# Kernel tuning notes

Hardware: AMD Instinct MI355X
Metric: run time of the kernel (lower is better)

Reference implementation:

```python
import jax, jax.numpy as jnp
import numpy as np

HEADS, DIM_HEAD = 8, 75            # Attention defaults in source
SCALE = DIM_HEAD ** -0.5
NUM_FOURIER = 64
PATCH = 4


def scale_norm(x, g, eps=1e-5):
    n = jnp.maximum(jnp.linalg.norm(x, axis=-1, keepdims=True), eps)
    return x / n * g


def attention(x, ctx, mask, wq, wkv, wo, bo):
    b, nq, _ = x.shape
    q = (x @ wq).reshape(b, nq, HEADS, DIM_HEAD)
    k, v = jnp.split(ctx @ wkv, 2, axis=-1)
    k = k.reshape(b, -1, HEADS, DIM_HEAD)
    v = v.reshape(b, -1, HEADS, DIM_HEAD)
    sim = jnp.einsum('bihd,bjhd->bhij', q, k) * SCALE
    if mask is not None:
        sim = jnp.where(mask[:, None, None, :], sim, -jnp.finfo(sim.dtype).max)
    a = jax.nn.softmax(sim, axis=-1)
    out = jnp.einsum('bhij,bjhd->bihd', a, v).reshape(b, nq, HEADS * DIM_HEAD)
    return out @ wo + bo


def feedforward(x, w1, b1, w2, b2):
    return jax.nn.gelu(x @ w1 + b1, approximate=False) @ w2 + b2


def fourier_encode(x, num_encodings):
    xu = x[..., None]
    scales = (2.0 ** jnp.arange(num_encodings)).astype(x.dtype)
    xs = xu / scales
    return jnp.concatenate([jnp.sin(xs), jnp.cos(xs), xu], axis=-1)


def sparsify(x, threshold=0.3):
    # x: (b, h, w, nt, c) patched volume. Fixed max_len = h*w*nt; stable sort
    # compacts kept voxels to the front in row-major (y,x,t) order, matching
    # torch.where ordering. Padded slots are zeroed and masked out.
    b, h, w, nt, c = x.shape
    N = h * w * nt
    mask = (jnp.abs(jnp.max(x, axis=-1)) > threshold).reshape(b, N)
    ys, xs, ts = jnp.meshgrid(jnp.arange(h), jnp.arange(w), jnp.arange(nt), indexing='ij')
    pos = jnp.stack([2.0 * ys / h - 1.0, 2.0 * xs / w - 1.0, 2.0 * ts / nt - 1.0], -1)
    pos = pos.reshape(N, 3).astype(x.dtype)
    order = jnp.argsort((~mask).astype(jnp.int32), axis=1)  # jax sort is stable
    mask_s = jnp.take_along_axis(mask, order, axis=1)
    pos_s = pos[order] * mask_s[..., None]
    vals_s = jnp.take_along_axis(x.reshape(b, N, c), order[..., None], axis=1) * mask_s[..., None]
    return pos_s, vals_s, mask_s


def _forward(input, latents, pos_emb,
             ca_g, ca_ctx_g, ca_q, ca_kv, ca_ow, ca_ob,
             cf_g, cf_w1, cf_b1, cf_w2, cf_b2,
             la_g, la_q, la_kv, la_ow, la_ob,
             lf_g, lf_w1, lf_b1, lf_w2, lf_b2,
             logits_w, logits_b):
    num_tbins = input.shape[0]
    x = jnp.transpose(input, (1, 3, 4, 0, 2))  # b h w t c
    b, H, W, t, c = x.shape
    p = PATCH
    x = x.reshape(b, H // p, p, W // p, p, t, c)
    x = jnp.transpose(x, (0, 1, 3, 5, 2, 4, 6)).reshape(b, H // p, W // p, t, p * p * c)
    pos, vals, mask = sparsify(x)
    enc = fourier_encode(pos, NUM_FOURIER)           # (b, N, 3, 2*nf+1)
    enc = enc.reshape(enc.shape[0], enc.shape[1], -1)
    data = jnp.concatenate([vals, enc], axis=-1)     # (b, N, input_dim)
    data = jax.lax.stop_gradient(data)               # torch builds it under no_grad
    lat = jnp.broadcast_to((latents + pos_emb)[None], (b,) + latents.shape)
    depth = ca_g.shape[0]
    for d in range(depth):
        lat = attention(scale_norm(lat, ca_g[d]), scale_norm(data, ca_ctx_g[d]), mask,
                        ca_q[d], ca_kv[d], ca_ow[d], ca_ob[d]) + lat
        lat = feedforward(scale_norm(lat, cf_g[d]), cf_w1[d], cf_b1[d], cf_w2[d], cf_b2[d]) + lat
        xn = scale_norm(lat, la_g[d])
        lat = attention(xn, xn, None, la_q[d], la_kv[d], la_ow[d], la_ob[d]) + lat
        lat = feedforward(scale_norm(lat, lf_g[d]), lf_w1[d], lf_b1[d], lf_w2[d], lf_b2[d]) + lat
    out = lat @ logits_w + logits_b                  # (b, num_latents, oc)
    n = out.shape[1] // num_tbins
    out = out.reshape(b, n, num_tbins, out.shape[-1])
    return jnp.transpose(out, (2, 0, 1, 3))          # (t, b, n, oc)


def setup_inputs() -> dict:
    key = jax.random.key(0)
    ks = jax.random.split(key, 16)
    D, LD, ID, IN, FF, NL, OC = 5, 512, 435, 600, 2048, 128, 64
    def rn(k, shape, scale=0.02):
        return jax.random.normal(k, shape, jnp.float32) * scale
    return {
        'input': jax.random.normal(ks[0], (8, 4, 3, 128, 128), jnp.float32),
        'latents': rn(ks[1], (NL, LD), 1.0),
        'pos_emb': rn(ks[2], (NL, LD), 1.0),
        'ca_g': jnp.ones((D,), jnp.float32),
        'ca_ctx_g': jnp.ones((D,), jnp.float32),
        'ca_q': rn(ks[3], (D, LD, IN)),
        'ca_kv': rn(ks[4], (D, ID, 2 * IN)),
        'ca_ow': rn(ks[5], (D, IN, LD)),
        'ca_ob': jnp.zeros((D, LD), jnp.float32),
        'cf_g': jnp.ones((D,), jnp.float32),
        'cf_w1': rn(ks[6], (D, LD, FF)),
        'cf_b1': jnp.zeros((D, FF), jnp.float32),
        'cf_w2': rn(ks[7], (D, FF, LD)),
        'cf_b2': jnp.zeros((D, LD), jnp.float32),
        'la_g': jnp.ones((D,), jnp.float32),
        'la_q': rn(ks[8], (D, LD, IN)),
        'la_kv': rn(ks[9], (D, LD, 2 * IN)),
        'la_ow': rn(ks[10], (D, IN, LD)),
        'la_ob': jnp.zeros((D, LD), jnp.float32),
        'lf_g': jnp.ones((D,), jnp.float32),
        'lf_w1': rn(ks[11], (D, LD, FF)),
        'lf_b1': jnp.zeros((D, FF), jnp.float32),
        'lf_w2': rn(ks[12], (D, FF, LD)),
        'lf_b2': jnp.zeros((D, LD), jnp.float32),
        'logits_w': rn(ks[13], (LD, OC)),
        'logits_b': jnp.zeros((OC,), jnp.float32),
    }


def reference(input, latents, pos_emb,
              ca_g, ca_ctx_g, ca_q, ca_kv, ca_ow, ca_ob,
              cf_g, cf_w1, cf_b1, cf_w2, cf_b2,
              la_g, la_q, la_kv, la_ow, la_ob,
              lf_g, lf_w1, lf_b1, lf_w2, lf_b2,
              logits_w, logits_b):
    return _forward(input, latents, pos_emb,
                    ca_g, ca_ctx_g, ca_q, ca_kv, ca_ow, ca_ob,
                    cf_g, cf_w1, cf_b1, cf_w2, cf_b2,
                    la_g, la_q, la_kv, la_ow, la_ob,
                    lf_g, lf_w1, lf_b1, lf_w2, lf_b2,
                    logits_w, logits_b)
```

## Files before the change

### kernel.cpp

```cpp
#include <hip/hip_runtime.h>
#include <math.h>

typedef unsigned short u16;
typedef long long ll;
typedef __attribute__((ext_vector_type(8))) short short8;
typedef __attribute__((ext_vector_type(4))) float f32x4;

#define TBINS 8
#define BATCH 4
#define CIN 3
#define WIMG 128
#define PC 48
#define NVOX 8192
#define ID 435
#define IDP 448
#define LD 512
#define INNER 600
#define INNERP 608
#define FFD 2048
#define NL 128
#define OC 64
#define DEPTH 5
#define HEADS 8
#define DH 75
#define DHP 96
#define BK 32
#define NCH 16
#define FCH 512
#define FKT 64
#define KVLD 1536
#define QLD 768
#define QKVLD 2304

static __device__ __forceinline__ u16 f2bf(float f) {
    unsigned x = __float_as_uint(f);
    unsigned r = (x + 0x7fffu + ((x >> 16) & 1u)) >> 16;
    return (u16)r;
}
static __device__ __forceinline__ float bf2f(u16 v) {
    return __uint_as_float(((unsigned)v) << 16);
}
static __device__ __forceinline__ void gload_lds16(const u16* g, u16* l) {
    __builtin_amdgcn_global_load_lds(
        (const __attribute__((address_space(1))) unsigned int*)g,
        (__attribute__((address_space(3))) unsigned int*)l, 16, 0, 0);
}

__global__ __launch_bounds__(256) void mask_kernel(const float* __restrict__ input,
                                                   unsigned char* __restrict__ mask) {
    int idx = blockIdx.x * 256 + threadIdx.x;
    if (idx >= BATCH * NVOX) return;
    int b = idx >> 13, i = idx & (NVOX - 1);
    int tt = i & 7, wx = (i >> 3) & 31, hy = i >> 8;
    float mx = -3.4e38f;
    for (int ch = 0; ch < PC; ++ch) {
        int py = ch / 12, px = (ch / 3) & 3, cc = ch % 3;
        float v = input[((size_t)((tt * BATCH + b) * CIN + cc) << 14) +
                        (hy * 4 + py) * WIMG + (wx * 4 + px)];
        mx = fmaxf(mx, v);
    }
    mask[idx] = (fabsf(mx) > 0.3f) ? 1 : 0;
}

__global__ __launch_bounds__(64) void compact_kernel(const unsigned char* __restrict__ mask,
                                                     int* __restrict__ perm,
                                                     int* __restrict__ Kc) {
    int b = blockIdx.x, lane = threadIdx.x;
    int offs = 0;
    for (int c = 0; c < NVOX / 64; ++c) {
        int i = c * 64 + lane;
        int m = mask[(b << 13) + i];
        unsigned long long bal = __ballot(m != 0);
        int excl = __popcll(bal & ((1ull << lane) - 1ull));
        if (m) perm[(b << 13) + offs + excl] = i;
        offs += __popcll(bal);
    }
    if (lane == 0) Kc[b] = offs;
}

__global__ __launch_bounds__(256) void build_all(const float* __restrict__ input,
                                                 const int* __restrict__ perm,
                                                 const int* __restrict__ Kc,
                                                 u16* __restrict__ normed) {
    int blk = blockIdx.x;
    int b = blk >> 13, r = blk & (NVOX - 1);
    int tid = threadIdx.x;
    u16* out = normed + (size_t)blk * IDP;
    int Kb = Kc[b];
    if (r >= Kb) {
        for (int e = tid; e < IDP; e += 256) out[e] = 0;
        return;
    }
    __shared__ float row[IDP];
    __shared__ float red[256];
    int i = perm[(b << 13) + r];
    int tt = i & 7, wx = (i >> 3) & 31, hy = i >> 8;
    float pos0 = 2.f * hy / 32.f - 1.f;
    float pos1 = 2.f * wx / 32.f - 1.f;
    float pos2 = 2.f * tt / 8.f - 1.f;
    for (int e = tid; e < IDP; e += 256) {
        float v = 0.f;
        if (e < PC) {
            int py = e / 12, px = (e / 3) & 3, cc = e % 3;
            v = input[((size_t)((tt * BATCH + b) * CIN + cc) << 14) +
                      (hy * 4 + py) * WIMG + (wx * 4 + px)];
        } else if (e < ID) {
            int e2 = e - PC;
            int dim = e2 / 129, rem = e2 - dim * 129;
            float pp = (dim == 0) ? pos0 : (dim == 1 ? pos1 : pos2);
            if (rem < 64)       v = sinf(ldexpf(pp, -rem));
            else if (rem < 128) v = cosf(ldexpf(pp, -(rem - 64)));
            else                v = pp;
        }
        row[e] = v;
    }
    __syncthreads();
    float ss = 0.f;
    for (int e = tid; e < ID; e += 256) ss += row[e] * row[e];
    red[tid] = ss; __syncthreads();
    for (int s = 128; s > 0; s >>= 1) { if (tid < s) red[tid] += red[tid + s]; __syncthreads(); }
    float scale = 1.f / fmaxf(sqrtf(red[0]), 1e-5f);
    for (int e = tid; e < IDP; e += 256) out[e] = f2bf(row[e] * scale);
}

__global__ __launch_bounds__(256) void lat_init(const float* __restrict__ latents,
                                                const float* __restrict__ pos_emb,
                                                float* __restrict__ lat) {
    int idx = blockIdx.x * 256 + threadIdx.x;
    if (idx >= BATCH * NL * LD) return;
    int rem = idx & (NL * LD - 1);
    lat[idx] = latents[rem] + pos_emb[rem];
}

__global__ __launch_bounds__(256) void scale_norm_bf(const float* __restrict__ x,
                                                     u16* __restrict__ o,
                                                     const float* __restrict__ g, int gi,
                                                     int cols) {
    int rowi = blockIdx.x, tid = threadIdx.x;
    const float* xr = x + (size_t)rowi * cols;
    u16* orow = o + (size_t)rowi * cols;
    __shared__ float red[256];
    float ss = 0.f;
    for (int c = tid; c < cols; c += 256) { float v = xr[c]; ss += v * v; }
    red[tid] = ss; __syncthreads();
    for (int s = 128; s > 0; s >>= 1) { if (tid < s) red[tid] += red[tid + s]; __syncthreads(); }
    float scale = g[gi] / fmaxf(sqrtf(red[0]), 1e-5f);
    for (int c = tid; c < cols; c += 256) orow[c] = f2bf(xr[c] * scale);
}

__global__ __launch_bounds__(256) void fill_kernel(float* __restrict__ p, long long n, float v) {
    long long idx = (long long)blockIdx.x * 256 + threadIdx.x;
    if (idx < n) p[idx] = v;
}

__global__ __launch_bounds__(256) void conv_bf(const float* __restrict__ src, u16* __restrict__ dst, int n) {
    int idx = blockIdx.x * 256 + threadIdx.x;
    if (idx < n) dst[idx] = f2bf(src[idx]);
}

struct TJobs {
    const float* src[11];
    u16* dst[11];
    int R[11], C[11], Rp[11], flag[11];
    int tstart[12];
    int njobs;
};
__global__ __launch_bounds__(256) void transpose_multi(TJobs J) {
    int bx = blockIdx.x;
    int j = 0;
    while (j + 1 < J.njobs && bx >= J.tstart[j + 1]) ++j;
    int lt = bx - J.tstart[j];
    int tilesX = J.Rp[j] >> 5;
    int tx = lt % tilesX, ty = lt / tilesX;
    const float* src = J.src[j];
    u16* dst = J.dst[j];
    int R = J.R[j], C = J.C[j], Rp = J.Rp[j], fl = J.flag[j];
    __shared__ float t[32][33];
    int bx0 = tx * 32, by0 = ty * 32;
    int ttx = threadIdx.x & 31, tty = threadIdx.x >> 5;
#pragma unroll
    for (int p = 0; p < 4; ++p) {
        int r = bx0 + tty + p * 8, c = by0 + ttx;
        t[tty + p * 8][ttx] = (r < R && c < C) ? src[(size_t)r * C + c] : 0.f;
    }
    __syncthreads();
#pragma unroll
    for (int p = 0; p < 4; ++p) {
        int c = by0 + tty + p * 8, r = bx0 + ttx;
        if (c < C && r < Rp) {
            int cp = c;
            if (fl == 1)      cp = (c / 75) * 96 + c % 75;
            else if (fl == 2) { int sec = c / 600, rem = c - sec * 600;
                                cp = sec * 768 + (rem / 75) * 96 + rem % 75; }
            dst[(size_t)cp * Rp + r] = f2bf(t[ttx][tty + p * 8]);
        }
    }
}

__global__ __launch_bounds__(256) void pack_vt_self(const u16* __restrict__ qkvs, u16* __restrict__ vt) {
    int idx = blockIdx.x * 256 + threadIdx.x;
    if (idx >= BATCH * HEADS * DH * NL) return;
    int l = idx & (NL - 1);
    int dd = (idx >> 7) % DH;
    int bh = idx / (DH * NL);
    int b = bh >> 3, h = bh & 7;
    vt[idx] = qkvs[(size_t)(b * NL + l) * QKVLD + 2 * QLD + h * DHP + dd];
}

__global__ __launch_bounds__(256) void softmax_u16(u16* __restrict__ S, int cols,
                                                   const int* __restrict__ Kc, int b0,
                                                   int rows_per_b) {
    int rowi = blockIdx.x, tid = threadIdx.x;
    u16* p = S + (size_t)rowi * cols;
    int lim = Kc ? Kc[b0 + rowi / rows_per_b] : cols;
    __shared__ float red[256];
    if (lim <= 0) { for (int j = tid; j < cols; j += 256) p[j] = 0; return; }
    float v[32];
    int nit = (lim + 255) >> 8;
    float mx = -3.4e38f;
    for (int s = 0; s < nit; ++s) {
        int j = s * 256 + tid;
        float x = (j < lim) ? bf2f(p[j]) : -3.4e38f;
        v[s] = x;
        mx = fmaxf(mx, x);
    }
    red[tid] = mx; __syncthreads();
    for (int s = 128; s > 0; s >>= 1) { if (tid < s) red[tid] = fmaxf(red[tid], red[tid + s]); __syncthreads(); }
    mx = red[0]; __syncthreads();
    float sum = 0.f;
    for (int s = 0; s < nit; ++s) {
        int j = s * 256 + tid;
        float e = (j < lim) ? expf(v[s] - mx) : 0.f;
        v[s] = e; sum += e;
    }
    red[tid] = sum; __syncthreads();
    for (int s = 128; s > 0; s >>= 1) { if (tid < s) red[tid] += red[tid + s]; __syncthreads(); }
    float inv = (red[0] > 0.f) ? 1.f / red[0] : 0.f;
    int nco = (cols + 255) >> 8;
    for (int s = 0; s < nco; ++s) {
        int j = s * 256 + tid;
        if (j < cols) p[j] = f2bf((s < nit && j < lim) ? v[s] * inv : 0.f);
    }
}

#define KS_LD 104
__global__ __launch_bounds__(256) void flash_ctx(
    const u16* __restrict__ qg,
    const u16* __restrict__ kvn,
    const int* __restrict__ Kc,
    float* __restrict__ Opart,
    float* __restrict__ mlb,
    float scale) {
    int ch = blockIdx.x, bh = blockIdx.y;
    int b = bh >> 3, h = bh & 7;
    int lim = Kc[b];
    int v0 = ch * FCH;
    int nval = min(FCH, lim - v0);
    int tid = threadIdx.x, wv = tid >> 6, lane = tid & 63;
    int fr = lane & 15, fc = lane >> 4;
    float* Op = Opart + ((size_t)bh * NCH + ch) * (128 * 80);
    float* mlp = mlb + ((size_t)bh * NCH + ch) * 256;
    if (nval <= 0) {
        for (int i = tid; i < 128 * 80; i += 256) Op[i] = 0.f;
        for (int i = tid; i < 128; i += 256) { mlp[2 * i] = -3.4e38f; mlp[2 * i + 1] = 0.f; }
        return;
    }
    __shared__ __align__(16) u16 Ks[FKT * KS_LD];
    __shared__ __align__(16) u16 Vt[80 * 72];
    __shared__ __align__(16) u16 Ps[4 * 32 * 72];
    const u16* kbase = kvn + ((size_t)b * NVOX) * KVLD + h * DHP;
    const u16* vbase = kbase + QLD;
    short8 qf[2][3];
    const u16* qb = qg + ((size_t)(b * NL) + wv * 32) * QLD + h * DHP;
#pragma unroll
    for (int i = 0; i < 2; ++i)
#pragma unroll
        for (int kk = 0; kk < 3; ++kk)
            qf[i][kk] = *(const short8*)(qb + (size_t)(i * 16 + fr) * QLD + kk * 32 + fc * 8);
    float m_run[2][4], l_run[2][4];
#pragma unroll
    for (int i = 0; i < 2; ++i)
#pragma unroll
        for (int r = 0; r < 4; ++r) { m_run[i][r] = -3.4e38f; l_run[i][r] = 0.f; }
    f32x4 o[2][5] = {};
    u16* Pw = Ps + wv * (32 * 72);
    int ktiles = (nval + FKT - 1) / FKT;
    for (int kt = 0; kt < ktiles; ++kt) {
        int kvox = v0 + kt * FKT;
        for (int t = 0; t < 3; ++t) {
            int idx = t * 256 + tid;
            int row = idx / 12, cc = idx - row * 12;
            short8 v = *(const short8*)(kbase + (size_t)(kvox + row) * KVLD + cc * 8);
            *(short8*)(Ks + row * KS_LD + cc * 8) = v;
        }
        for (int t = 0; t < 3; ++t) {
            int idx = t * 256 + tid;
            if (idx < 640) {
                int row = idx / 10, c8 = idx - row * 10;
                short8 v = *(const short8*)(vbase + (size_t)(kvox + row) * KVLD + c8 * 8);
#pragma unroll
                for (int e = 0; e < 8; ++e)
                    Vt[(c8 * 8 + e) * 72 + row] = (u16)v[e];
            }
        }
        __syncthreads();
        f32x4 sc[2][4] = {};
#pragma unroll
        for (int kk = 0; kk < 3; ++kk) {
            short8 bf[4];
#pragma unroll
            for (int j = 0; j < 4; ++j)
                bf[j] = *(const short8*)(Ks + (j * 16 + fr) * KS_LD + kk * 32 + fc * 8);
#pragma unroll
            for (int i = 0; i < 2; ++i)
#pragma unroll
                for (int j = 0; j < 4; ++j)
                    sc[i][j] = __builtin_amdgcn_mfma_f32_16x16x32_bf16(qf[i][kk], bf[j], sc[i][j], 0, 0, 0);
        }
        float alpha[2][4];
#pragma unroll
        for (int i = 0; i < 2; ++i) {
#pragma unroll
            for (int r = 0; r < 4; ++r) {
                float mt = -3.4e38f;
#pragma unroll
                for (int j = 0; j < 4; ++j) {
                    int cl = kt * FKT + j * 16 + fr;
                    float s = (cl < nval) ? sc[i][j][r] * scale : -3.4e38f;
                    sc[i][j][r] = s;
                    mt = fmaxf(mt, s);
                }
                for (int sft = 1; sft < 16; sft <<= 1) mt = fmaxf(mt, __shfl_xor(mt, sft, 16));
                float mn = fmaxf(m_run[i][r], mt);
                float al = __expf(m_run[i][r] - mn);
                m_run[i][r] = mn;
                float lt = 0.f;
#pragma unroll
                for (int j = 0; j < 4; ++j) {
                    float p = __expf(sc[i][j][r] - mn);
                    sc[i][j][r] = p;
                    lt += p;
                }
                for (int sft = 1; sft < 16; sft <<= 1) lt += __shfl_xor(lt, sft, 16);
                l_run[i][r] = l_run[i][r] * al + lt;
                alpha[i][r] = al;
            }
        }
#pragma unroll
        for (int i = 0; i < 2; ++i)
#pragma unroll
            for (int j = 0; j < 4; ++j)
#pragma unroll
                for (int r = 0; r < 4; ++r)
                    Pw[(i * 16 + fc * 4 + r) * 72 + j * 16 + fr] = f2bf(sc[i][j][r]);
#pragma unroll
        for (int i = 0; i < 2; ++i)
#pragma unroll
            for (int n = 0; n < 5; ++n)
#pragma unroll
                for (int r = 0; r < 4; ++r)
                    o[i][n][r] *= alpha[i][r];
        __syncthreads();
#pragma unroll
        for (int kk = 0; kk < 2; ++kk) {
            short8 pf[2], vf[5];
#pragma unroll
            for (int i = 0; i < 2; ++i)
                pf[i] = *(const short8*)(Pw + (i * 16 + fr) * 72 + kk * 32 + fc * 8);
#pragma unroll
            for (int n = 0; n < 5; ++n)
                vf[n] = *(const short8*)(Vt + (n * 16 + fr) * 72 + kk * 32 + fc * 8);
#pragma unroll
            for (int i = 0; i < 2; ++i)
#pragma unroll
                for (int n = 0; n < 5; ++n)
                    o[i][n] = __builtin_amdgcn_mfma_f32_16x16x32_bf16(pf[i], vf[n], o[i][n], 0, 0, 0);
        }
        __syncthreads();
    }
#pragma unroll
    for (int i = 0; i < 2; ++i) {
#pragma unroll
        for (int n = 0; n < 5; ++n)
#pragma unroll
            for (int r = 0; r < 4; ++r) {
                int row = wv * 32 + i * 16 + fc * 4 + r;
                Op[row * 80 + n * 16 + fr] = o[i][n][r];
            }
        if (fr == 0) {
#pragma unroll
            for (int r = 0; r < 4; ++r) {
                int row = wv * 32 + i * 16 + fc * 4 + r;
                mlp[2 * row] = m_run[i][r];
                mlp[2 * row + 1] = l_run[i][r];
            }
        }
    }
}

__global__ __launch_bounds__(128) void combine_ctx(const float* __restrict__ Opart,
                                                   const float* __restrict__ mlb,
                                                   u16* __restrict__ attn_bf) {
    int blk = blockIdx.x;
    int bh = blk >> 7, row = blk & 127;
    int b = bh >> 3, h = bh & 7;
    int tid = threadIdx.x;
    float mc[NCH], lc[NCH];
    float mstar = -3.4e38f;
    for (int c = 0; c < NCH; ++c) {
        const float* mlp = mlb + ((size_t)bh * NCH + c) * 256 + 2 * row;
        mc[c] = mlp[0]; lc[c] = mlp[1];
        mstar = fmaxf(mstar, mc[c]);
    }
    float L = 0.f;
    float wc[NCH];
    for (int c = 0; c < NCH; ++c) {
        float ww = __expf(mc[c] - mstar);
        wc[c] = ww; L += ww * lc[c];
    }
    float invL = (L > 0.f) ? 1.f / L : 0.f;
    if (tid < DH) {
        float s = 0.f;
        for (int c = 0; c < NCH; ++c)
            s += Opart[(((size_t)bh * NCH + c) * 128 + row) * 80 + tid] * wc[c];
        attn_bf[((size_t)(b * 128 + row)) * INNERP + h * DH + tid] = f2bf(s * invL);
    }
    if (h == 7 && tid >= DH && tid < DH + (INNERP - INNER))
        attn_bf[((size_t)(b * 128 + row)) * INNERP + INNER + (tid - DH)] = 0;
}

__global__ __launch_bounds__(256) void gemm_bf16(
    const u16* __restrict__ A, const u16* __restrict__ B, void* __restrict__ Dv,
    const float* __restrict__ alphaPtr, int alphaIdx, float alphaConst,
    int M, int N, int K, int lda, int ldb, int ldd, int nh,
    ll sAo, ll sAi, ll sBo, ll sBi, ll sDo, ll sDi,
    int splitK, int mode, const float* __restrict__ bias, float biasScale, int act) {
    __shared__ __align__(16) u16 As[128 * BK];
    __shared__ __align__(16) u16 Bs[128 * BK];
    const int tid = threadIdx.x;
    int zb = blockIdx.z / splitK, kc = blockIdx.z - zb * splitK;
    int zo = zb / nh, zi = zb - zo * nh;
    const u16* Ab = A + (size_t)zo * sAo + (size_t)zi * sAi;
    const u16* Bb = B + (size_t)zo * sBo + (size_t)zi * sBi;
    const int bm = blockIdx.x * 128, bn = blockIdx.y * 128;
    int nk = K >> 5;
    int per = (nk + splitK - 1) / splitK;
    int k0 = kc * per * BK;
    int k1 = min(K, k0 + per * BK);

    const int wv = tid >> 6, lane = tid & 63;
    const int wm = (wv & 1) << 6, wn = (wv >> 1) << 6;
    const int fr = lane & 15, fc = lane >> 4;
    f32x4 acc[4][4] = {};

    const int lr = lane >> 2, lc = (lane & 3) << 3;
    const u16* ga0 = Ab + (size_t)(bm + wv * 16 + lr) * lda + k0 + lc;
    const u16* ga1 = ga0 + (size_t)64 * lda;
    const u16* gb0 = Bb + (size_t)(bn + wv * 16 + lr) * ldb + k0 + lc;
    const u16* gb1 = gb0 + (size_t)64 * ldb;
    u16* la0 = As + (wv * 16) * BK;
    u16* la1 = As + (wv * 16 + 64) * BK;
    u16* lb0 = Bs + (wv * 16) * BK;
    u16* lb1 = Bs + (wv * 16 + 64) * BK;

    for (int kb = k0; kb < k1; kb += BK) {
        gload_lds16(ga0, la0);
        gload_lds16(ga1, la1);
        gload_lds16(gb0, lb0);
        gload_lds16(gb1, lb1);
        ga0 += BK; ga1 += BK; gb0 += BK; gb1 += BK;
        __syncthreads();
        short8 af[4], bfr[4];
#pragma unroll
        for (int i = 0; i < 4; ++i)
            af[i] = *(const short8*)(As + (wm + i * 16 + fr) * BK + fc * 8);
#pragma unroll
        for (int j = 0; j < 4; ++j)
            bfr[j] = *(const short8*)(Bs + (wn + j * 16 + fr) * BK + fc * 8);
#pragma unroll
        for (int i = 0; i < 4; ++i)
#pragma unroll
            for (int j = 0; j < 4; ++j)
                acc[i][j] = __builtin_amdgcn_mfma_f32_16x16x32_bf16(af[i], bfr[j], acc[i][j], 0, 0, 0);
        __syncthreads();
    }
    float alpha = alphaConst * (alphaPtr ? alphaPtr[alphaIdx] : 1.f);
    if (mode == 6) {
        float* Do = (float*)Dv;
#pragma unroll
        for (int i = 0; i < 4; ++i)
#pragma unroll
            for (int j = 0; j < 4; ++j) {
                int gn = bn + wn + j * 16 + fr;
                if (gn >= N) continue;
                float bv = bias ? bias[gn] * biasScale : 0.f;
                int gm0 = bm + wm + i * 16 + fc * 4;
#pragma unroll
                for (int r = 0; r < 4; ++r) {
                    int gm = gm0 + r;
                    if (gm >= M) continue;
                    int b = gm >> 7, l = gm & 127;
                    int tt = l & 7, nn = l >> 3;
                    atomicAdd(&Do[(((size_t)(tt * BATCH + b)) * 16 + nn) * 64 + gn],
                              acc[i][j][r] * alpha + bv);
                }
            }
        return;
    }
    float* Db = (float*)Dv + (size_t)zo * sDo + (size_t)zi * sDi;
    u16* Du = (u16*)Dv + (size_t)zo * sDo + (size_t)zi * sDi;
#pragma unroll
    for (int i = 0; i < 4; ++i) {
#pragma unroll
        for (int j = 0; j < 4; ++j) {
            int gn = bn + wn + j * 16 + fr;
            if (gn >= N) continue;
            float bv = bias ? bias[gn] * biasScale : 0.f;
            int gm0 = bm + wm + i * 16 + fc * 4;
#pragma unroll
            for (int r = 0; r < 4; ++r) {
                int gm = gm0 + r;
                if (gm >= M) continue;
                float v = acc[i][j][r] * alpha + bv;
                if (act) v = 0.5f * v * (1.f + erff(v * 0.70710678118654752f));
                size_t di = (size_t)gm * ldd + gn;
                if (mode == 2) Du[di] = f2bf(v);
                else           atomicAdd(&Db[di], v);
            }
        }
    }
}

extern "C" void kernel_launch(void* const* d_in, const int* in_sizes, int n_in,
                              void* d_out, int out_size, void* d_ws, size_t ws_size,
                              hipStream_t stream) {
    const float* input    = (const float*)d_in[0];
    const float* latents  = (const float*)d_in[1];
    const float* pos_emb  = (const float*)d_in[2];
    const float* ca_g     = (const float*)d_in[3];
    const float* ca_ctx_g = (const float*)d_in[4];
    const float* ca_q     = (const float*)d_in[5];
    const float* ca_kv    = (const float*)d_in[6];
    const float* ca_ow    = (const float*)d_in[7];
    const float* ca_ob    = (const float*)d_in[8];
    const float* cf_g     = (const float*)d_in[9];
    const float* cf_w1    = (const float*)d_in[10];
    const float* cf_b1    = (const float*)d_in[11];
    const float* cf_w2    = (const float*)d_in[12];
    const float* cf_b2    = (const float*)d_in[13];
    const float* la_g     = (const float*)d_in[14];
    const float* la_q     = (const float*)d_in[15];
    const float* la_kv    = (const float*)d_in[16];
    const float* la_ow    = (const float*)d_in[17];
    const float* la_ob    = (const float*)d_in[18];
    const float* lf_g     = (const float*)d_in[19];
    const float* lf_w1    = (const float*)d_in[20];
    const float* lf_b1    = (const float*)d_in[21];
    const float* lf_w2    = (const float*)d_in[22];
    const float* lf_b2    = (const float*)d_in[23];
    const float* logits_w = (const float*)d_in[24];
    const float* logits_b = (const float*)d_in[25];
    float* out = (float*)d_out;
    (void)ws_size; (void)n_in; (void)in_sizes; (void)out_size;

    char* w = (char*)d_ws;
    auto alloc = [&](size_t bytes) { void* p = (void*)w; w += (bytes + 255) & ~(size_t)255; return p; };
    int* perm        = (int*)alloc((size_t)BATCH * NVOX * 4);
    int* Kc          = (int*)alloc(64);
    unsigned char* mask = (unsigned char*)alloc((size_t)BATCH * NVOX);
    float* lat       = (float*)alloc((size_t)BATCH * NL * LD * 4);
    u16* latn_bf     = (u16*)alloc((size_t)BATCH * NL * LD * 2);
    u16* qg          = (u16*)alloc((size_t)BATCH * NL * QLD * 2);
    u16* qkvs        = (u16*)alloc((size_t)BATCH * NL * QKVLD * 2);
    u16* attn_bf     = (u16*)alloc((size_t)BATCH * NL * INNERP * 2);
    u16* ffb_bf      = (u16*)alloc((size_t)BATCH * NL * FFD * 2);
    u16* vs_t        = (u16*)alloc((size_t)BATCH * HEADS * DH * NL * 2);
    alloc(64 * 1024);
    u16* wqp_t   = (u16*)alloc((size_t)QLD * LD * 2);
    u16* wkv_t   = (u16*)alloc((size_t)KVLD * IDP * 2);
    u16* wlqkv_t = (u16*)alloc((size_t)QKVLD * LD * 2);
    size_t padw_f32 = ((size_t)QLD * LD + (size_t)KVLD * IDP + (size_t)QKVLD * LD) / 2;
    u16* wow_t   = (u16*)alloc((size_t)LD * INNERP * 2);
    u16* wf1_t   = (u16*)alloc((size_t)FFD * LD * 2);
    u16* wf2_t   = (u16*)alloc((size_t)LD * FFD * 2);
    u16* wlow_t  = (u16*)alloc((size_t)LD * INNERP * 2);
    u16* wlf1_t  = (u16*)alloc((size_t)FFD * LD * 2);
    u16* wlf2_t  = (u16*)alloc((size_t)LD * FFD * 2);
    u16* wlog_t  = (u16*)alloc((size_t)OC * LD * 2);
    u16* normed  = (u16*)alloc((size_t)BATCH * NVOX * IDP * 2);
    u16* E       = (u16*)alloc((size_t)2 * 1024 * 1024);
    u16* kvn     = (u16*)alloc((size_t)BATCH * NVOX * KVLD * 2);
    alloc((size_t)64 * 1024);
    float* Opart = (float*)alloc((size_t)32 * NCH * 128 * 80 * 4);
    float* mlb   = (float*)alloc((size_t)32 * NCH * 128 * 2 * 4);

    const float scaleS = 1.0f / sqrtf((float)DH);
    const int M4 = BATCH * NL;

    auto G = [&](const u16* A, const u16* B, void* D, const float* aP, int aI, float aC,
                 int M, int N, int K, int lda, int ldb, int ldd, int nh, int nb,
                 ll sAo, ll sAi, ll sBo, ll sBi, ll sDo, ll sDi,
                 int splitK, int mode, const float* bias = nullptr, float biasScale = 1.f,
                 int act = 0) {
        dim3 g((M + 127) / 128, (N + 127) / 128, nb * splitK);
        hipLaunchKernelGGL(gemm_bf16, g, dim3(256), 0, stream, A, B, D, aP, aI, aC,
                           M, N, K, lda, ldb, ldd, nh, sAo, sAi, sBo, sBi, sDo, sDi,
                           splitK, mode, bias, biasScale, act);
    };

    hipLaunchKernelGGL(mask_kernel, dim3((BATCH * NVOX + 255) / 256), dim3(256), 0, stream, input, mask);
    hipLaunchKernelGGL(compact_kernel, dim3(BATCH), dim3(64), 0, stream, mask, perm, Kc);
    hipLaunchKernelGGL(lat_init, dim3((BATCH * NL * LD + 255) / 256), dim3(256), 0, stream, latents, pos_emb, lat);
    hipLaunchKernelGGL(fill_kernel, dim3(((ll)padw_f32 + 255) / 256), dim3(256), 0, stream,
                       (float*)wqp_t, (ll)padw_f32, 0.f);
    hipLaunchKernelGGL(build_all, dim3(BATCH * NVOX), dim3(256), 0, stream, input, perm, Kc, normed);

    for (int d = 0; d < DEPTH; ++d) {
        TJobs J;
        int t = 0;
        auto addJob = [&](const float* s, u16* ds, int R, int C, int Rp, int fl) {
            J.src[t] = s; J.dst[t] = ds; J.R[t] = R; J.C[t] = C; J.Rp[t] = Rp; J.flag[t] = fl;
            J.tstart[t] = (t == 0) ? 0 : J.tstart[t - 1] +
                          (J.Rp[t - 1] >> 5) * ((J.C[t - 1] + 31) >> 5);
            ++t;
        };
        addJob(ca_q  + (size_t)d * LD * INNER,     wqp_t,   LD,  INNER,     LD,     1);
        addJob(ca_kv + (size_t)d * ID * 2 * INNER, wkv_t,   ID,  2 * INNER, IDP,    2);
        addJob(ca_ow + (size_t)d * INNER * LD,     wow_t,   INNER, LD,      INNERP, 0);
        addJob(cf_w1 + (size_t)d * LD * FFD,       wf1_t,   LD,  FFD,       LD,     0);
        addJob(cf_w2 + (size_t)d * FFD * LD,       wf2_t,   FFD, LD,        FFD,    0);
        addJob(la_q  + (size_t)d * LD * INNER,     wlqkv_t, LD,  INNER,     LD,     1);
        addJob(la_kv + (size_t)d * LD * 2 * INNER, wlqkv_t + (size_t)QLD * LD, LD, 2 * INNER, LD, 2);
        addJob(la_ow + (size_t)d * INNER * LD,     wlow_t,  INNER, LD,      INNERP, 0);
        addJob(lf_w1 + (size_t)d * LD * FFD,       wlf1_t,  LD,  FFD,       LD,     0);
        addJob(lf_w2 + (size_t)d * FFD * LD,       wlf2_t,  FFD, LD,        FFD,    0);
        if (d == 0) addJob(logits_w,               wlog_t,  LD,  OC,        LD,     0);
        J.njobs = t;
        J.tstart[t] = J.tstart[t - 1] + (J.Rp[t - 1] >> 5) * ((J.C[t - 1] + 31) >> 5);
        hipLaunchKernelGGL(transpose_multi, dim3(J.tstart[t]), dim3(256), 0, stream, J);

        hipLaunchKernelGGL(scale_norm_bf, dim3(M4), dim3(256), 0, stream, lat, latn_bf, ca_g, d, LD);
        G(latn_bf, wqp_t, qg, nullptr, 0, 1.f, M4, QLD, LD, LD, LD, QLD, 1, 1,
          0, 0, 0, 0, 0, 0, 1, 2);
        G(normed, wkv_t, kvn, ca_ctx_g, d, 1.f, BATCH * NVOX, KVLD, IDP, IDP, IDP, KVLD, 1, 1,
          0, 0, 0, 0, 0, 0, 1, 2);
        hipLaunchKernelGGL(flash_ctx, dim3(NCH, 32), dim3(256), 0, stream,
                           qg, kvn, Kc, Opart, mlb, scaleS);
        hipLaunchKernelGGL(combine_ctx, dim3(32 * 128), dim3(128), 0, stream, Opart, mlb, attn_bf);
        G(attn_bf, wow_t, lat, nullptr, 0, 1.f, M4, LD, INNERP, INNERP, INNERP, LD, 1, 1,
          0, 0, 0, 0, 0, 0, 2, 1, ca_ob + (size_t)d * LD, 0.5f);

        hipLaunchKernelGGL(scale_norm_bf, dim3(M4), dim3(256), 0, stream, lat, latn_bf, cf_g, d, LD);
        G(latn_bf, wf1_t, ffb_bf, nullptr, 0, 1.f, M4, FFD, LD, LD, LD, FFD, 1, 1,
          0, 0, 0, 0, 0, 0, 1, 2, cf_b1 + (size_t)d * FFD, 1.f, 1);
        G(ffb_bf, wf2_t, lat, nullptr, 0, 1.f, M4, LD, FFD, FFD, FFD, LD, 1, 1,
          0, 0, 0, 0, 0, 0, 8, 1, cf_b2 + (size_t)d * LD, 0.125f);

        hipLaunchKernelGGL(scale_norm_bf, dim3(M4), dim3(256), 0, stream, lat, latn_bf, la_g, d, LD);
        G(latn_bf, wlqkv_t, qkvs, nullptr, 0, 1.f, M4, QKVLD, LD, LD, LD, QKVLD, 1, 1,
          0, 0, 0, 0, 0, 0, 1, 2);
        hipLaunchKernelGGL(pack_vt_self, dim3((BATCH * HEADS * DH * NL + 255) / 256), dim3(256), 0, stream,
                           qkvs, vs_t);
        G(qkvs, qkvs + QLD, E, nullptr, 0, scaleS, NL, NL, DHP, QKVLD, QKVLD, NL, 8, 32,
          (ll)NL * QKVLD, (ll)DHP, (ll)NL * QKVLD, (ll)DHP,
          (ll)HEADS * NL * NL, (ll)NL * NL, 1, 2);
        hipLaunchKernelGGL(softmax_u16, dim3(BATCH * HEADS * NL), dim3(256), 0, stream,
                           E, NL, (const int*)nullptr, 0, HEADS * NL);
        G(E, vs_t, attn_bf, nullptr, 0, 1.f, NL, DH, NL, NL, NL, INNERP, 8, 32,
          (ll)HEADS * NL * NL, (ll)NL * NL, (ll)HEADS * DH * NL, (ll)DH * NL,
          (ll)NL * INNERP, (ll)DH, 1, 2);
        G(attn_bf, wlow_t, lat, nullptr, 0, 1.f, M4, LD, INNERP, INNERP, INNERP, LD, 1, 1,
          0, 0, 0, 0, 0, 0, 2, 1, la_ob + (size_t)d * LD, 0.5f);

        hipLaunchKernelGGL(scale_norm_bf, dim3(M4), dim3(256), 0, stream, lat, latn_bf, lf_g, d, LD);
        G(latn_bf, wlf1_t, ffb_bf, nullptr, 0, 1.f, M4, FFD, LD, LD, LD, FFD, 1, 1,
          0, 0, 0, 0, 0, 0, 1, 2, lf_b1 + (size_t)d * FFD, 1.f, 1);
        G(ffb_bf, wlf2_t, lat, nullptr, 0, 1.f, M4, LD, FFD, FFD, FFD, LD, 1, 1,
          0, 0, 0, 0, 0, 0, 8, 1, lf_b2 + (size_t)d * LD, 0.125f);
    }

    hipLaunchKernelGGL(conv_bf, dim3((M4 * LD + 255) / 256), dim3(256), 0, stream, lat, latn_bf, M4 * LD);
    hipLaunchKernelGGL(fill_kernel, dim3((TBINS * BATCH * 16 * OC + 255) / 256), dim3(256), 0, stream,
                       out, (ll)TBINS * BATCH * 16 * OC, 0.f);
    G(latn_bf, wlog_t, out, nullptr, 0, 1.f, M4, OC, LD, LD, LD, 0, 1, 1,
      0, 0, 0, 0, 0, 0, 4, 6, logits_b, 0.25f);
}
```

Baseline: 2.131 ms.

## Transpose MFMA operands for row-contiguous epilogue stores and swap grid axes

Swaps the A/B operands of the MFMA so each lane holds four consecutive output columns of one row instead of four rows of one column. This lets the bf16 epilogue write 4 packed values with one 8-byte store, and makes the fp32 atomic adds hit contiguous addresses. The grid is also reordered so blockIdx.x walks N tiles, which changes which tiles run together and may affect L2 reuse of A tiles. The vector path only runs when ldd, N and the strides are multiples of 4, with a scalar fallback otherwise.

```diff
diff --git a/kernel.cpp b/kernel.cpp
--- a/kernel.cpp
+++ b/kernel.cpp
@@ -4,6 +4,7 @@
 typedef unsigned short u16;
 typedef long long ll;
 typedef __attribute__((ext_vector_type(8))) short short8;
+typedef __attribute__((ext_vector_type(4))) short short4v;
 typedef __attribute__((ext_vector_type(4))) float f32x4;
 
 #define TBINS 8
@@ -442,7 +443,7 @@
     int zo = zb / nh, zi = zb - zo * nh;
     const u16* Ab = A + (size_t)zo * sAo + (size_t)zi * sAi;
     const u16* Bb = B + (size_t)zo * sBo + (size_t)zi * sBi;
-    const int bm = blockIdx.x * 128, bn = blockIdx.y * 128;
+    const int bm = blockIdx.y * 128, bn = blockIdx.x * 128;
     int nk = K >> 5;
     int per = (nk + splitK - 1) / splitK;
     int k0 = kc * per * BK;
@@ -481,51 +482,64 @@
         for (int i = 0; i < 4; ++i)
 #pragma unroll
             for (int j = 0; j < 4; ++j)
-                acc[i][j] = __builtin_amdgcn_mfma_f32_16x16x32_bf16(af[i], bfr[j], acc[i][j], 0, 0, 0);
+                acc[i][j] = __builtin_amdgcn_mfma_f32_16x16x32_bf16(bfr[j], af[i], acc[i][j], 0, 0, 0);
         __syncthreads();
     }
     float alpha = alphaConst * (alphaPtr ? alphaPtr[alphaIdx] : 1.f);
     if (mode == 6) {
         float* Do = (float*)Dv;
 #pragma unroll
-        for (int i = 0; i < 4; ++i)
+        for (int i = 0; i < 4; ++i) {
+            int gm = bm + wm + i * 16 + fr;
+            if (gm >= M) continue;
+            int b = gm >> 7, l = gm & 127;
+            int tt = l & 7, nn = l >> 3;
+            size_t obase = (((size_t)(tt * BATCH + b)) * 16 + nn) * 64;
 #pragma unroll
             for (int j = 0; j < 4; ++j) {
-                int gn = bn + wn + j * 16 + fr;
-                if (gn >= N) continue;
-                float bv = bias ? bias[gn] * biasScale : 0.f;
-                int gm0 = bm + wm + i * 16 + fc * 4;
+                int gn0 = bn + wn + j * 16 + fc * 4;
 #pragma unroll
                 for (int r = 0; r < 4; ++r) {
-                    int gm = gm0 + r;
-                    if (gm >= M) continue;
-                    int b = gm >> 7, l = gm & 127;
-                    int tt = l & 7, nn = l >> 3;
-                    atomicAdd(&Do[(((size_t)(tt * BATCH + b)) * 16 + nn) * 64 + gn],
-                              acc[i][j][r] * alpha + bv);
+                    int gn = gn0 + r;
+                    if (gn >= N) continue;
+                    float bv = bias ? bias[gn] * biasScale : 0.f;
+                    atomicAdd(&Do[obase + gn], acc[i][j][r] * alpha + bv);
                 }
             }
+        }
         return;
     }
     float* Db = (float*)Dv + (size_t)zo * sDo + (size_t)zi * sDi;
     u16* Du = (u16*)Dv + (size_t)zo * sDo + (size_t)zi * sDi;
+    int vec4 = (mode == 2) && (((unsigned)(ldd | N | (int)(sDi & 3) | (int)(sDo & 3)) & 3u) == 0u);
 #pragma unroll
     for (int i = 0; i < 4; ++i) {
+        int gm = bm + wm + i * 16 + fr;
+        if (gm >= M) continue;
 #pragma unroll
         for (int j = 0; j < 4; ++j) {
-            int gn = bn + wn + j * 16 + fr;
-            if (gn >= N) continue;
-            float bv = bias ? bias[gn] * biasScale : 0.f;
-            int gm0 = bm + wm + i * 16 + fc * 4;
-#pragma unroll
-            for (int r = 0; r < 4; ++r) {
-                int gm = gm0 + r;
-                if (gm >= M) continue;
-                float v = acc[i][j][r] * alpha + bv;
-                if (act) v = 0.5f * v * (1.f + erff(v * 0.70710678118654752f));
-                size_t di = (size_t)gm * ldd + gn;
-                if (mode == 2) Du[di] = f2bf(v);
-                else           atomicAdd(&Db[di], v);
+            int gn0 = bn + wn + j * 16 + fc * 4;
+            if (vec4) {
+                if (gn0 >= N) continue;
+                short4v pk;
+#pragma unroll
+                for (int r = 0; r < 4; ++r) {
+                    float v = acc[i][j][r] * alpha + (bias ? bias[gn0 + r] * biasScale : 0.f);
+                    if (act) v = 0.5f * v * (1.f + erff(v * 0.70710678118654752f));
+                    pk[r] = (short)f2bf(v);
+                }
+                *(short4v*)(Du + (size_t)gm * ldd + gn0) = pk;
+            } else {
+#pragma unroll
+                for (int r = 0; r < 4; ++r) {
+                    int gn = gn0 + r;
+                    if (gn >= N) continue;
+                    float v = acc[i][j][r] * alpha + (bias ? bias[gn] * biasScale : 0.f);
+                    if (act) v = 0.5f * v * (1.f + erff(v * 0.70710678118654752f));
+                    size_t di = (size_t)gm * ldd + gn;
+                    if (mode == 2) Du[di] = f2bf(v);
+                    else           atomicAdd(&Db[di], v);
+                }
             }
         }
     }
@@ -602,7 +616,7 @@
                  ll sAo, ll sAi, ll sBo, ll sBi, ll sDo, ll sDi,
                  int splitK, int mode, const float* bias = nullptr, float biasScale = 1.f,
                  int act = 0) {
-        dim3 g((M + 127) / 128, (N + 127) / 128, nb * splitK);
+        dim3 g((N + 127) / 128, (M + 127) / 128, nb * splitK);
         hipLaunchKernelGGL(gemm_bf16, g, dim3(256), 0, stream, A, B, D, aP, aI, aC,
                            M, N, K, lda, ldb, ldd, nh, sAo, sAi, sBo, sBi, sDo, sDi,
                            splitK, mode, bias, biasScale, act);
```

Measured after the change: 2.588 ms. 21.4% more time.
